# Kernel optimization log

Measured on AMD Instinct MI355X. Metric: run time of the kernel, lower is better.

## Reference

```python
import jax, jax.numpy as jnp
import numpy as np

N, E, FEAT, DIM, B = 200000, 1600000, 128, 64, 256


def setup_inputs() -> dict:
    key = jax.random.key(0)
    ks = jax.random.split(key, 16)
    s = 0.05
    x = jax.random.normal(ks[0], (N, FEAT), jnp.float32)
    edge_index = jax.random.randint(ks[1], (2, E), 0, N)
    batch = jnp.sort(jax.random.randint(ks[2], (N,), 0, B))
    return {
        'x': x,
        'edge_index': edge_index,
        'batch': batch,
        'lin0_w': jax.random.normal(ks[3], (FEAT, DIM), jnp.float32) * s,
        'lin0_b': jax.random.normal(ks[4], (DIM,), jnp.float32) * s,
        'conv_w': jax.random.normal(ks[5], (DIM, DIM), jnp.float32) * s,
        'conv_b': jax.random.normal(ks[6], (DIM,), jnp.float32) * s,
        'gru_w_ih': jax.random.normal(ks[7], (3 * DIM, DIM), jnp.float32) * s,
        'gru_w_hh': jax.random.normal(ks[8], (3 * DIM, DIM), jnp.float32) * s,
        'gru_b_ih': jax.random.normal(ks[9], (3 * DIM,), jnp.float32) * s,
        'gru_b_hh': jax.random.normal(ks[10], (3 * DIM,), jnp.float32) * s,
        'lstm_w_ih': jax.random.normal(ks[11], (4 * DIM, 2 * DIM), jnp.float32) * s,
        'lstm_w_hh': jax.random.normal(ks[12], (4 * DIM, DIM), jnp.float32) * s,
        'lstm_b_ih': jax.random.normal(ks[13], (4 * DIM,), jnp.float32) * s,
        'lstm_b_hh': jax.random.normal(ks[14], (4 * DIM,), jnp.float32) * s,
    }


def reference(x, edge_index, batch, lin0_w, lin0_b, conv_w, conv_b,
              gru_w_ih, gru_w_hh, gru_b_ih, gru_b_hh,
              lstm_w_ih, lstm_w_hh, lstm_b_ih, lstm_b_hh):
    n = x.shape[0]
    d = lin0_w.shape[1]
    # --- GCN normalization with self-loops (PyG gcn_norm, symmetric) ---
    loops = jnp.arange(n)
    row = jnp.concatenate([edge_index[0], loops])  # source nodes
    col = jnp.concatenate([edge_index[1], loops])  # target nodes
    deg = jax.ops.segment_sum(jnp.ones(row.shape, jnp.float32), col, num_segments=N)
    dinv = jnp.where(deg > 0, jax.lax.rsqrt(deg), 0.0)
    norm = dinv[row] * dinv[col]  # [E+N]

    out = jax.nn.relu(x @ lin0_w + lin0_b)  # [N, D]
    h = out  # GRU hidden (layer dim squeezed)
    feat = out
    for _ in range(3):
        # GCNConv: aggregate normalized neighbor messages
        hw = out @ conv_w                                   # [N, D]
        m = jax.ops.segment_sum(norm[:, None] * hw[row], col, num_segments=N) + conv_b
        m = jax.nn.relu(m)
        # torch.nn.GRU cell (gate order: reset, update, new)
        gi = m @ gru_w_ih.T + gru_b_ih
        gh = h @ gru_w_hh.T + gru_b_hh
        ir, iz, in_ = jnp.split(gi, 3, axis=-1)
        hr, hz, hn = jnp.split(gh, 3, axis=-1)
        r = jax.nn.sigmoid(ir + hr)
        z = jax.nn.sigmoid(iz + hz)
        ncand = jnp.tanh(in_ + r * hn)
        h = (1.0 - z) * ncand + z * h
        out = h
        feat = out

    # --- Set2Set pooling, processing_steps=3 (LSTM: 2D -> D) ---
    q_star = jnp.zeros((B, 2 * d), x.dtype)
    hl = jnp.zeros((B, d), x.dtype)
    cl = jnp.zeros((B, d), x.dtype)
    for _ in range(3):
        gates = q_star @ lstm_w_ih.T + lstm_b_ih + hl @ lstm_w_hh.T + lstm_b_hh
        i_, f_, g_, o_ = jnp.split(gates, 4, axis=-1)  # torch order i,f,g,o
        cl = jax.nn.sigmoid(f_) * cl + jax.nn.sigmoid(i_) * jnp.tanh(g_)
        hl = jax.nn.sigmoid(o_) * jnp.tanh(cl)
        q = hl                                             # [B, D]
        e = jnp.sum(out * q[batch], axis=-1)               # [N]
        emax = jax.ops.segment_max(e, batch, num_segments=B)
        a = jnp.exp(e - jax.lax.stop_gradient(emax)[batch])
        denom = jax.ops.segment_sum(a, batch, num_segments=B)
        a = a / denom[batch]                               # scatter-softmax
        r_read = jax.ops.segment_sum(a[:, None] * out, batch, num_segments=B)
        q_star = jnp.concatenate([q, r_read], axis=-1)     # [B, 2D]
    return (q_star, feat)
```

## Files before the change

kernel.cpp:

```cpp
#include <hip/hip_runtime.h>
#include <math.h>

#define FEATD 128
#define DIM 64
#define NB 256
#define SCB 256
#define KB 16
#define RNG 128
#define NBUCKMAX 2048
#define CH1 8192

typedef short bf16x8 __attribute__((ext_vector_type(8)));
typedef float f32x4 __attribute__((ext_vector_type(4)));

__device__ __forceinline__ float frcp_(float x){ return __builtin_amdgcn_rcpf(x); }
__device__ __forceinline__ float sigmoidf_(float x){ return frcp_(1.f+__expf(-x)); }
__device__ __forceinline__ float tanhf_(float x){ float e=__expf(2.f*x); return 1.f-2.f*frcp_(e+1.f); }

__device__ __forceinline__ unsigned short f2bf(float f){
  unsigned u = __float_as_uint(f);
  unsigned r = (u + 0x7FFFu + ((u>>16)&1u)) >> 16;
  return (unsigned short)r;
}
__device__ __forceinline__ float bf2f(unsigned short s){
  return __uint_as_float(((unsigned)s)<<16);
}

__device__ __forceinline__ int lower_bound_i(const int* __restrict__ a, int n, int key){
  int lo=0, hi=n;
  while(lo<hi){ int mid=(lo+hi)>>1; if(a[mid]<key) lo=mid+1; else hi=mid; }
  return lo;
}

__global__ void k_count(const int* __restrict__ col, int* __restrict__ deg, int E){
  int i=blockIdx.x*blockDim.x+threadIdx.x;
  if(i<E) atomicAdd(&deg[col[i]],1);
}

__global__ void k_dinv(const int* __restrict__ deg, float* __restrict__ dinv, int n){
  int i=blockIdx.x*blockDim.x+threadIdx.x;
  if(i<n) dinv[i]=rsqrtf((float)(deg[i]+1));
}

__global__ __launch_bounds__(256) void k_scan_part(const int* __restrict__ deg, int* __restrict__ part, int n){
  __shared__ int s[256];
  int b=blockIdx.x;
  int chunk=(n+SCB-1)/SCB;
  int lo=b*chunk, hi=min(lo+chunk,n);
  int acc=0;
  for(int i=lo+threadIdx.x;i<hi;i+=256) acc+=deg[i];
  s[threadIdx.x]=acc; __syncthreads();
  for(int off=128;off;off>>=1){
    if(threadIdx.x<off) s[threadIdx.x]+=s[threadIdx.x+off];
    __syncthreads();
  }
  if(threadIdx.x==0) part[b]=s[0];
}

__global__ __launch_bounds__(256) void k_scan_mid(int* __restrict__ part){
  __shared__ int s[256];
  int t=threadIdx.x;
  s[t]=part[t]; __syncthreads();
  for(int off=1;off<256;off<<=1){
    int v=(t>=off)? s[t-off]:0;
    __syncthreads();
    s[t]+=v;
    __syncthreads();
  }
  part[t]=(t>0)? s[t-1]:0;
}

__global__ __launch_bounds__(256) void k_scan_out(const int* __restrict__ deg, const int* __restrict__ part,
                                                  int* __restrict__ rp, int* __restrict__ gcur, int n){
  __shared__ int s[256];
  int b=blockIdx.x, t=threadIdx.x;
  int chunk=(n+SCB-1)/SCB;
  int lo=b*chunk, hi=min(lo+chunk,n);
  int tchunk=(chunk+255)/256;
  int tlo=lo+t*tchunk, thi=min(tlo+tchunk,hi);
  int acc=0;
  for(int i=tlo;i<thi;i++) acc+=deg[i];
  s[t]=acc; __syncthreads();
  for(int off=1;off<256;off<<=1){
    int v=(t>=off)? s[t-off]:0;
    __syncthreads();
    s[t]+=v;
    __syncthreads();
  }
  int pre=part[b]+((t>0)? s[t-1]:0);
  for(int i=tlo;i<thi;i++){
    rp[i]=pre;
    if((i&(RNG-1))==0) gcur[(i>>7)*32]=pre;
    pre+=deg[i];
  }
  if(b==SCB-1 && t==0) rp[n]=part[b]+s[255];
}

__global__ __launch_bounds__(256) void k_binscat(const int* __restrict__ row, const int* __restrict__ col,
                       int* __restrict__ gcur, unsigned* __restrict__ tmp, int E, int nbuck){
  __shared__ int lcnt[NBUCKMAX];
  __shared__ int lcur[NBUCKMAX];
  int t=threadIdx.x;
  for(int i=t;i<nbuck;i+=256) lcnt[i]=0;
  __syncthreads();
  int lo=blockIdx.x*CH1, hi=min(lo+CH1,E);
  for(int i=lo+t;i<hi;i+=256) atomicAdd(&lcnt[col[i]>>7],1);
  __syncthreads();
  for(int i=t;i<nbuck;i+=256){
    int cnt=lcnt[i];
    lcur[i]=(cnt>0)? atomicAdd(&gcur[i*32],cnt):0;
  }
  __syncthreads();
  for(int i=lo+t;i<hi;i+=256){
    int c=col[i], r=row[i];
    int pos=atomicAdd(&lcur[c>>7],1);
    tmp[pos]=((unsigned)r<<7)|(unsigned)(c&127);
  }
}

__global__ __launch_bounds__(256) void k_place(const unsigned* __restrict__ tmp, const int* __restrict__ rp,
                      const float* __restrict__ dinv, int2* __restrict__ epack, int n, int nbuck){
  __shared__ int lfill[RNG];
  __shared__ int lrp[RNG];
  __shared__ float ldv[RNG];
  int b=blockIdx.x, t=threadIdx.x;
  int nbase=b*RNG;
  int nn=min(RNG,n-nbase);
  if(t<nn){ lfill[t]=0; lrp[t]=rp[nbase+t]; ldv[t]=dinv[nbase+t]; }
  __syncthreads();
  int lo=rp[nbase], hi=rp[min(nbase+RNG,n)];
  for(int j=lo+t;j<hi;j+=256){
    unsigned v=tmp[j];
    int cl=v&127;
    int r=(int)(v>>7);
    int pos=atomicAdd(&lfill[cl],1);
    epack[lrp[cl]+pos]=make_int2(r,__float_as_int(dinv[r]*ldv[cl]));
  }
}

__global__ void k_prep_plain(const float* __restrict__ W, unsigned short* __restrict__ Bf, int K, int C){
  int i=blockIdx.x*blockDim.x+threadIdx.x;
  if(i>=K*C) return;
  int k=i/C, c=i%C;
  int t=c>>4, s=k>>5, lane=(c&15)|(((k>>3)&3)<<4), r=k&7;
  int S=K>>5;
  Bf[(((t*S)+s)*64+lane)*8+r]=f2bf(W[(size_t)k*C+c]);
}

__global__ void k_prep_gru(const float* __restrict__ wih, const float* __restrict__ whh,
                           unsigned short* __restrict__ Bf){
  int i=blockIdx.x*blockDim.x+threadIdx.x;
  if(i>=128*256) return;
  int k=i>>8, c=i&255;
  float v;
  if(c<128){
    v = (k<64) ? wih[c*64+k] : whh[c*64+(k-64)];
  } else if(c<192){
    v = (k<64) ? wih[c*64+k] : 0.f;
  } else {
    v = (k<64) ? 0.f : whh[(c-64)*64+(k-64)];
  }
  int t=c>>4, s=k>>5, lane=(c&15)|(((k>>3)&3)<<4), r=k&7;
  Bf[(((s*16)+t)*64+lane)*8+r]=f2bf(v);
}

__global__ __launch_bounds__(256) void k_lin0(const float* __restrict__ x, const unsigned short* __restrict__ Bf,
                      const float* __restrict__ bias,
                      unsigned short* __restrict__ hb, int ngrp){
  __shared__ __align__(16) unsigned short lt[4][16][72];
  int l=threadIdx.x&63, w=threadIdx.x>>6;
  int g=blockIdx.x*4+w;
  if(g>=ngrp) return;
  int row16=l&15, koff=(l>>4)*8, l16=l&15;
  f32x4 acc[4]={};
  const float* xr = x + (size_t)(g*16+row16)*128 + koff;
  #pragma unroll
  for(int s=0;s<4;s++){
    f32x4 a0=*(const f32x4*)(xr+s*32);
    f32x4 a1=*(const f32x4*)(xr+s*32+4);
    bf16x8 af;
    #pragma unroll
    for(int r=0;r<4;r++){ af[r]=(short)f2bf(a0[r]); af[4+r]=(short)f2bf(a1[r]); }
    #pragma unroll
    for(int t=0;t<4;t++){
      bf16x8 bf=*(const bf16x8*)(Bf+(((t*4)+s)*64+l)*8);
      acc[t]=__builtin_amdgcn_mfma_f32_16x16x32_bf16(af,bf,acc[t],0,0,0);
    }
  }
  #pragma unroll
  for(int t=0;t<4;t++){
    int c=t*16+l16;
    float b=bias[c];
    #pragma unroll
    for(int j=0;j<4;j++)
      lt[w][(l>>4)*4+j][c]=f2bf(fmaxf(acc[t][j]+b,0.f));
  }
  #pragma unroll
  for(int i=0;i<4;i++){
    int rl=i*4+(l>>4);
    uint2 v=*(const uint2*)&lt[w][rl][l16*4];
    ((uint2*)hb)[(((unsigned)(g*16+rl))<<4)+l16]=v;
  }
}

__global__ __launch_bounds__(256,4) void k_gruagg(
                     const unsigned short* __restrict__ hin, unsigned short* __restrict__ hout,
                     const int* __restrict__ rp, const int2* __restrict__ epack,
                     const float* __restrict__ dinv,
                     const unsigned short* __restrict__ Bcnv, const float* __restrict__ cb,
                     const unsigned short* __restrict__ Bgru,
                     const float* __restrict__ bih, const float* __restrict__ bhh,
                     float* __restrict__ h, int last, int ngrp, int n){
  __shared__ __align__(16) unsigned short Bs[8192];
  __shared__ __align__(16) unsigned short tAH[4][2][16][72];
  int tid=threadIdx.x;
  int l=tid&63, w=tid>>6;
  int g=blockIdx.x*4+w;
  bool act = g<ngrp;
  int gc = act? g : (ngrp-1);
  int q=l>>4, l16=l&15;
  int row16=l&15, koff=(l>>4)*8;

  unsigned short (*tA)[72] = tAH[w][0];
  unsigned short (*tH)[72] = tAH[w][1];

  bf16x8 bc[8];
  #pragma unroll
  for(int f=0;f<8;f++) bc[f]=*(const bf16x8*)(Bcnv+((size_t)f*64+l)*8);

  {
    const f32x4* gh=(const f32x4*)Bgru; f32x4* lh=(f32x4*)Bs;
    #pragma unroll
    for(int i=0;i<4;i++) lh[i*256+tid]=gh[i*256+tid];
  }

  const uint2* h64=(const uint2*)hin;
  #pragma unroll
  for(int rr=0;rr<4;rr++){
    int node=min(gc*16+rr*4+q, n-1);
    float a0=0.f,a1=0.f,a2=0.f,a3=0.f, b0=0.f,b1=0.f,b2=0.f,b3=0.f;
    int s=rp[node], e=rp[node+1];
    uint2 selfp=h64[((unsigned)node<<4)+l16];
    int j=s;
    for(; j+7<e; j+=8){
      int2 e0=epack[j],   e1=epack[j+1], e2=epack[j+2], e3=epack[j+3];
      int2 e4=epack[j+4], e5=epack[j+5], e6=epack[j+6], e7=epack[j+7];
      uint2 p0=h64[((unsigned)e0.x<<4)+l16];
      uint2 p1=h64[((unsigned)e1.x<<4)+l16];
      uint2 p2=h64[((unsigned)e2.x<<4)+l16];
      uint2 p3=h64[((unsigned)e3.x<<4)+l16];
      uint2 p4=h64[((unsigned)e4.x<<4)+l16];
      uint2 p5=h64[((unsigned)e5.x<<4)+l16];
      uint2 p6=h64[((unsigned)e6.x<<4)+l16];
      uint2 p7=h64[((unsigned)e7.x<<4)+l16];
      float n0=__int_as_float(e0.y), n1=__int_as_float(e1.y);
      float n2=__int_as_float(e2.y), n3=__int_as_float(e3.y);
      float n4=__int_as_float(e4.y), n5=__int_as_float(e5.y);
      float n6=__int_as_float(e6.y), n7=__int_as_float(e7.y);
      a0+=n0*bf2f((unsigned short)p0.x); a1+=n0*bf2f((unsigned short)(p0.x>>16));
      a2+=n0*bf2f((unsigned short)p0.y); a3+=n0*bf2f((unsigned short)(p0.y>>16));
      b0+=n1*bf2f((unsigned short)p1.x); b1+=n1*bf2f((unsigned short)(p1.x>>16));
      b2+=n1*bf2f((unsigned short)p1.y); b3+=n1*bf2f((unsigned short)(p1.y>>16));
      a0+=n2*bf2f((unsigned short)p2.x); a1+=n2*bf2f((unsigned short)(p2.x>>16));
      a2+=n2*bf2f((unsigned short)p2.y); a3+=n2*bf2f((unsigned short)(p2.y>>16));
      b0+=n3*bf2f((unsigned short)p3.x); b1+=n3*bf2f((unsigned short)(p3.x>>16));
      b2+=n3*bf2f((unsigned short)p3.y); b3+=n3*bf2f((unsigned short)(p3.y>>16));
      a0+=n4*bf2f((unsigned short)p4.x); a1+=n4*bf2f((unsigned short)(p4.x>>16));
      a2+=n4*bf2f((unsigned short)p4.y); a3+=n4*bf2f((unsigned short)(p4.y>>16));
      b0+=n5*bf2f((unsigned short)p5.x); b1+=n5*bf2f((unsigned short)(p5.x>>16));
      b2+=n5*bf2f((unsigned short)p5.y); b3+=n5*bf2f((unsigned short)(p5.y>>16));
      a0+=n6*bf2f((unsigned short)p6.x); a1+=n6*bf2f((unsigned short)(p6.x>>16));
      a2+=n6*bf2f((unsigned short)p6.y); a3+=n6*bf2f((unsigned short)(p6.y>>16));
      b0+=n7*bf2f((unsigned short)p7.x); b1+=n7*bf2f((unsigned short)(p7.x>>16));
      b2+=n7*bf2f((unsigned short)p7.y); b3+=n7*bf2f((unsigned short)(p7.y>>16));
    }
    for(; j+3<e; j+=4){
      int2 e0=epack[j];
      int2 e1=epack[j+1];
      int2 e2=epack[j+2];
      int2 e3=epack[j+3];
      uint2 p0=h64[((unsigned)e0.x<<4)+l16];
      uint2 p1=h64[((unsigned)e1.x<<4)+l16];
      uint2 p2=h64[((unsigned)e2.x<<4)+l16];
      uint2 p3=h64[((unsigned)e3.x<<4)+l16];
      float n0=__int_as_float(e0.y), n1=__int_as_float(e1.y);
      float n2=__int_as_float(e2.y), n3=__int_as_float(e3.y);
      a0+=n0*bf2f((unsigned short)p0.x); a1+=n0*bf2f((unsigned short)(p0.x>>16));
      a2+=n0*bf2f((unsigned short)p0.y); a3+=n0*bf2f((unsigned short)(p0.y>>16));
      b0+=n1*bf2f((unsigned short)p1.x); b1+=n1*bf2f((unsigned short)(p1.x>>16));
      b2+=n1*bf2f((unsigned short)p1.y); b3+=n1*bf2f((unsigned short)(p1.y>>16));
      a0+=n2*bf2f((unsigned short)p2.x); a1+=n2*bf2f((unsigned short)(p2.x>>16));
      a2+=n2*bf2f((unsigned short)p2.y); a3+=n2*bf2f((unsigned short)(p2.y>>16));
      b0+=n3*bf2f((unsigned short)p3.x); b1+=n3*bf2f((unsigned short)(p3.x>>16));
      b2+=n3*bf2f((unsigned short)p3.y); b3+=n3*bf2f((unsigned short)(p3.y>>16));
    }
    for(; j+1<e; j+=2){
      int2 e0=epack[j];
      int2 e1=epack[j+1];
      uint2 p0=h64[((unsigned)e0.x<<4)+l16];
      uint2 p1=h64[((unsigned)e1.x<<4)+l16];
      float n0=__int_as_float(e0.y), n1=__int_as_float(e1.y);
      a0+=n0*bf2f((unsigned short)p0.x); a1+=n0*bf2f((unsigned short)(p0.x>>16));
      a2+=n0*bf2f((unsigned short)p0.y); a3+=n0*bf2f((unsigned short)(p0.y>>16));
      b0+=n1*bf2f((unsigned short)p1.x); b1+=n1*bf2f((unsigned short)(p1.x>>16));
      b2+=n1*bf2f((unsigned short)p1.y); b3+=n1*bf2f((unsigned short)(p1.y>>16));
    }
    if(j<e){
      int2 e0=epack[j];
      uint2 p0=h64[((unsigned)e0.x<<4)+l16];
      float n0=__int_as_float(e0.y);
      a0+=n0*bf2f((unsigned short)p0.x); a1+=n0*bf2f((unsigned short)(p0.x>>16));
      a2+=n0*bf2f((unsigned short)p0.y); a3+=n0*bf2f((unsigned short)(p0.y>>16));
    }
    float dv=dinv[node]; dv*=dv;
    a0+=b0+dv*bf2f((unsigned short)selfp.x);
    a1+=b1+dv*bf2f((unsigned short)(selfp.x>>16));
    a2+=b2+dv*bf2f((unsigned short)selfp.y);
    a3+=b3+dv*bf2f((unsigned short)(selfp.y>>16));
    int ri=rr*4+q;
    unsigned* tAp=(unsigned*)&tA[ri][l16*4];
    tAp[0]=(unsigned)f2bf(a0)|(((unsigned)f2bf(a1))<<16);
    tAp[1]=(unsigned)f2bf(a2)|(((unsigned)f2bf(a3))<<16);
    unsigned* tHp=(unsigned*)&tH[ri][l16*4];
    tHp[0]=selfp.x; tHp[1]=selfp.y;
  }

  f32x4 accm[4]={};
  #pragma unroll
  for(int s=0;s<2;s++){
    bf16x8 af=*(const bf16x8*)&tA[row16][s*32+koff];
    #pragma unroll
    for(int t=0;t<4;t++)
      accm[t]=__builtin_amdgcn_mfma_f32_16x16x32_bf16(af,bc[t*2+s],accm[t],0,0,0);
  }
  #pragma unroll
  for(int t=0;t<4;t++){
    int c=t*16+l16;
    float b=cb[c];
    #pragma unroll
    for(int j=0;j<4;j++)
      tA[(l>>4)*4+j][c]=f2bf(fmaxf(accm[t][j]+b,0.f));
  }

  f32x4 acc[16]={};
  __syncthreads();
  #pragma unroll
  for(int s=0;s<4;s++){
    if(s>0){
      __syncthreads();
      const f32x4* gh=(const f32x4*)(Bgru+(size_t)s*8192); f32x4* lh=(f32x4*)Bs;
      #pragma unroll
      for(int i=0;i<4;i++) lh[i*256+tid]=gh[i*256+tid];
      __syncthreads();
    }
    bf16x8 af;
    if(s<2) af=*(const bf16x8*)&tA[row16][s*32+koff];
    else    af=*(const bf16x8*)&tH[row16][(s-2)*32+koff];
    #pragma unroll
    for(int t=0;t<16;t++){
      bf16x8 bf=*(const bf16x8*)(Bs+((size_t)t*64+l)*8);
      acc[t]=__builtin_amdgcn_mfma_f32_16x16x32_bf16(af,bf,acc[t],0,0,0);
    }
  }

  if(!act) return;
  float hn[16];
  #pragma unroll
  for(int t=0;t<4;t++){
    int d=t*16+l16;
    float br =bih[d]    +bhh[d];
    float bz =bih[64+d] +bhh[64+d];
    float bni=bih[128+d];
    float bnh=bhh[128+d];
    #pragma unroll
    for(int j=0;j<4;j++){
      float r  = sigmoidf_(acc[t][j]   + br);
      float z  = sigmoidf_(acc[4+t][j] + bz);
      float nc = tanhf_(acc[8+t][j] + bni + r*(acc[12+t][j] + bnh));
      float hold=bf2f(tH[(l>>4)*4+j][d]);
      hn[t*4+j]=(1.f-z)*nc + z*hold;
    }
  }
  #pragma unroll
  for(int t=0;t<4;t++){
    int d=t*16+l16;
    #pragma unroll
    for(int j=0;j<4;j++)
      tH[(l>>4)*4+j][d]=f2bf(hn[t*4+j]);
  }
  #pragma unroll
  for(int i=0;i<4;i++){
    int rl=i*4+(l>>4);
    uint2 v=*(const uint2*)&tH[rl][l16*4];
    ((uint2*)hout)[(((unsigned)(gc*16+rl))<<4)+l16]=v;
  }
  if(last){
    float* ft=(float*)&tAH[w][0][0][0];
    #pragma unroll
    for(int t=0;t<4;t++){
      int d=t*16+l16;
      #pragma unroll
      for(int j=0;j<4;j++)
        ft[((l>>4)*4+j)*68+d]=hn[t*4+j];
    }
    #pragma unroll
    for(int i=0;i<4;i++){
      int rl=i*4+(l>>4);
      f32x4 v=*(const f32x4*)&ft[rl*68+l16*4];
      *(f32x4*)&h[(size_t)(gc*16+rl)*64+l16*4]=v;
    }
  }
}

__global__ __launch_bounds__(256) void k_attn_part(const unsigned short* __restrict__ hb, const int* __restrict__ batch,
                        const float* __restrict__ hl, float* __restrict__ apart, int n){
  int b=blockIdx.x/KB, kb=blockIdx.x%KB;
  int tid=threadIdx.x, lane=tid&63, w=tid>>6;
  __shared__ float qs[64];
  __shared__ float wm[4], wsm[4];
  __shared__ float wacc[4][64];
  if(tid<64) qs[tid]=hl[b*64+tid];
  int lo=lower_bound_i(batch,n,b), hi=lower_bound_i(batch,n,b+1);
  int cnt=hi-lo;
  int chunk=(cnt+KB-1)/KB;
  int slo=lo+kb*chunk, shi=min(slo+chunk,hi);
  __syncthreads();
  float q=qs[lane];
  float mw=-3.0e38f, sw=0.f, aw=0.f;
  for(int i=slo+w;i<shi;i+=4){
    float f=bf2f(hb[(size_t)i*64+lane]);
    float v=f*q;
    #pragma unroll
    for(int off=32;off;off>>=1) v+=__shfl_xor(v,off);
    if(v>mw){
      float sc=__expf(mw-v);
      sw=sw*sc+1.f;
      aw=aw*sc+f;
      mw=v;
    } else {
      float p=__expf(v-mw);
      sw+=p;
      aw+=p*f;
    }
  }
  if(lane==0){ wm[w]=mw; wsm[w]=sw; }
  wacc[w][lane]=aw;
  __syncthreads();
  if(w==0){
    float M=fmaxf(fmaxf(wm[0],wm[1]),fmaxf(wm[2],wm[3]));
    float S=0.f, A=0.f;
    #pragma unroll
    for(int k=0;k<4;k++){
      float sc=__expf(wm[k]-M);
      S+=wsm[k]*sc;
      A+=wacc[k][lane]*sc;
    }
    float* p=apart+(size_t)blockIdx.x*68;
    p[lane]=A;
    if(lane==0){ p[64]=M; p[65]=S; }
  }
}

__global__ __launch_bounds__(256) void k_merge_lstm(const float* __restrict__ apart,
                   float* __restrict__ qstar, float* __restrict__ hl, float* __restrict__ cl,
                   const float* __restrict__ wih, const float* __restrict__ whh,
                   const float* __restrict__ bih, const float* __restrict__ bhh,
                   int do_merge, int do_lstm){
  int b=blockIdx.x, tid=threadIdx.x;
  __shared__ float qs[128];
  __shared__ float gates[256];
  if(do_merge){
    if(tid<64){
      const float* p0=apart+(size_t)b*KB*68;
      float M=-3.0e38f;
      #pragma unroll
      for(int k=0;k<KB;k++) M=fmaxf(M,p0[k*68+64]);
      float S=0.f, A=0.f;
      #pragma unroll
      for(int k=0;k<KB;k++){
        float sc=__expf(p0[k*68+64]-M);
        S+=p0[k*68+65]*sc;
        A+=p0[k*68+tid]*sc;
      }
      float inv=(S>0.f)? 1.f/S:0.f;
      float r=A*inv;
      qs[64+tid]=r;
      qstar[b*128+64+tid]=r;
    }
  } else {
    if(tid<64) qs[64+tid]=qstar[b*128+64+tid];
  }
  if(tid<64) qs[tid]=hl[b*64+tid];
  __syncthreads();
  if(!do_lstm) return;
  float acc=bih[tid]+bhh[tid];
  const float* wi=wih+(size_t)tid*128;
  #pragma unroll 8
  for(int k=0;k<128;k++) acc+=qs[k]*wi[k];
  const float* w2=whh+(size_t)tid*64;
  #pragma unroll 8
  for(int k=0;k<64;k++) acc+=qs[k]*w2[k];
  gates[tid]=acc;
  __syncthreads();
  if(tid<64){
    float i_=gates[tid], f_=gates[64+tid], g_=gates[128+tid], o_=gates[192+tid];
    float c=sigmoidf_(f_)*cl[b*64+tid]+sigmoidf_(i_)*tanhf(g_);
    float hn=sigmoidf_(o_)*tanhf(c);
    cl[b*64+tid]=c; hl[b*64+tid]=hn;
    qstar[b*128+tid]=hn;
  }
}

extern "C" void kernel_launch(void* const* d_in, const int* in_sizes, int n_in,
                              void* d_out, int out_size, void* d_ws, size_t ws_size,
                              hipStream_t stream){
  const float* x      =(const float*)d_in[0];
  const int*   ei     =(const int*)d_in[1];
  const int*   batch  =(const int*)d_in[2];
  const float* lin0_w =(const float*)d_in[3];
  const float* lin0_b =(const float*)d_in[4];
  const float* conv_w =(const float*)d_in[5];
  const float* conv_b =(const float*)d_in[6];
  const float* gwih   =(const float*)d_in[7];
  const float* gwhh   =(const float*)d_in[8];
  const float* gbih   =(const float*)d_in[9];
  const float* gbhh   =(const float*)d_in[10];
  const float* lwih   =(const float*)d_in[11];
  const float* lwhh   =(const float*)d_in[12];
  const float* lbih   =(const float*)d_in[13];
  const float* lbhh   =(const float*)d_in[14];

  int N = in_sizes[0]/FEATD;
  int E = in_sizes[1]/2;
  const int* row = ei;
  const int* col = ei + E;

  float* qstar = (float*)d_out;
  float* h     = (float*)d_out + NB*2*DIM;

  char* ws=(char*)d_ws;
  size_t off=0;
  auto alloc=[&](size_t bytes)->void*{ void* p=ws+off; off=(off+bytes+255)&~(size_t)255; return p; };
  int*   deg  =(int*)  alloc((size_t)N*4);
  float* dinv =(float*)alloc((size_t)N*4);
  int*   rp   =(int*)  alloc((size_t)(N+1)*4);
  int*   part =(int*)  alloc((size_t)SCB*4);
  int*   gcur =(int*)  alloc((size_t)NBUCKMAX*32*4);
  unsigned* tmp=(unsigned*)alloc((size_t)E*4);
  int2*  epack=(int2*) alloc((size_t)E*8);
  unsigned short* hb0  =(unsigned short*)alloc((size_t)N*64*2);
  unsigned short* hb1  =(unsigned short*)alloc((size_t)N*64*2);
  float* hl   =(float*)alloc((size_t)NB*DIM*4);
  float* cl   =(float*)alloc((size_t)NB*DIM*4);
  float* apart=(float*)alloc((size_t)NB*KB*68*4);
  unsigned short* Bgru =(unsigned short*)alloc(128*256*2);
  unsigned short* Blin =(unsigned short*)alloc(128*64*2);
  unsigned short* Bcnv =(unsigned short*)alloc(64*64*2);

  hipMemsetAsync(deg ,0,(size_t)N*4,stream);
  hipMemsetAsync(hl  ,0,(size_t)NB*DIM*4,stream);
  hipMemsetAsync(cl  ,0,(size_t)NB*DIM*4,stream);
  hipMemsetAsync(qstar,0,(size_t)NB*2*DIM*4,stream);

  int nbuck=(N+RNG-1)/RNG;

  k_count<<<(E+255)/256,256,0,stream>>>(col,deg,E);
  k_dinv <<<(N+255)/256,256,0,stream>>>(deg,dinv,N);
  k_scan_part<<<SCB,256,0,stream>>>(deg,part,N);
  k_scan_mid <<<1,256,0,stream>>>(part);
  k_scan_out <<<SCB,256,0,stream>>>(deg,part,rp,gcur,N);
  k_binscat<<<(E+CH1-1)/CH1,256,0,stream>>>(row,col,gcur,tmp,E,nbuck);
  k_place<<<nbuck,256,0,stream>>>(tmp,rp,dinv,epack,N,nbuck);

  k_prep_plain<<<(128*64+255)/256,256,0,stream>>>(lin0_w,Blin,128,64);
  k_prep_plain<<<(64*64+255)/256,256,0,stream>>>(conv_w,Bcnv,64,64);
  k_prep_gru  <<<(128*256+255)/256,256,0,stream>>>(gwih,gwhh,Bgru);

  int ngrp=(N+15)/16;
  int gb=(ngrp+3)/4;

  k_lin0<<<gb,256,0,stream>>>(x,Blin,lin0_b,hb0,ngrp);

  k_gruagg<<<gb,256,0,stream>>>(hb0,hb1,rp,epack,dinv,Bcnv,conv_b,Bgru,gbih,gbhh,h,0,ngrp,N);
  k_gruagg<<<gb,256,0,stream>>>(hb1,hb0,rp,epack,dinv,Bcnv,conv_b,Bgru,gbih,gbhh,h,0,ngrp,N);
  k_gruagg<<<gb,256,0,stream>>>(hb0,hb1,rp,epack,dinv,Bcnv,conv_b,Bgru,gbih,gbhh,h,1,ngrp,N);

  k_merge_lstm<<<NB,256,0,stream>>>(apart,qstar,hl,cl,lwih,lwhh,lbih,lbhh,0,1);
  for(int st=0;st<3;st++){
    k_attn_part<<<NB*KB,256,0,stream>>>(hb1,batch,hl,apart,N);
    int do_lstm = (st<2)? 1:0;
    k_merge_lstm<<<NB,256,0,stream>>>(apart,qstar,hl,cl,lwih,lwhh,lbih,lbhh,1,do_lstm);
  }
}
```

Measured before the change: 541.5 us.

## Restructure GRU GEMM by output tile to cut registers and raise occupancy

The fused aggregation+GRU kernel now computes gate outputs one 16-column tile at a time: the GRU weights are re-laid out so each tile's r/z/n gates sit in consecutive chunks, and the LDS staging buffer is halved. This drops the 16 live accumulator vectors to 4, moves the conv weight loads into a scoped block, and raises launch bounds from 4 to 6 waves per SIMD to improve latency hiding in the gather phase. It also folds the dinv computation into the scan-partition kernel, removing one launch. The cost is twice as many block-wide syncs and reloads of LDS weight chunks (8 stages instead of 4).

```diff
diff --git a/kernel.cpp b/kernel.cpp
--- a/kernel.cpp
+++ b/kernel.cpp
@@ -37,18 +37,18 @@
   if(i<E) atomicAdd(&deg[col[i]],1);
 }
 
-__global__ void k_dinv(const int* __restrict__ deg, float* __restrict__ dinv, int n){
-  int i=blockIdx.x*blockDim.x+threadIdx.x;
-  if(i<n) dinv[i]=rsqrtf((float)(deg[i]+1));
-}
-
-__global__ __launch_bounds__(256) void k_scan_part(const int* __restrict__ deg, int* __restrict__ part, int n){
+__global__ __launch_bounds__(256) void k_scan_part(const int* __restrict__ deg, int* __restrict__ part,
+                                                   float* __restrict__ dinv, int n){
   __shared__ int s[256];
   int b=blockIdx.x;
   int chunk=(n+SCB-1)/SCB;
   int lo=b*chunk, hi=min(lo+chunk,n);
   int acc=0;
-  for(int i=lo+threadIdx.x;i<hi;i+=256) acc+=deg[i];
+  for(int i=lo+threadIdx.x;i<hi;i+=256){
+    int d=deg[i];
+    acc+=d;
+    dinv[i]=rsqrtf((float)(d+1));
+  }
   s[threadIdx.x]=acc; __syncthreads();
   for(int off=128;off;off>>=1){
     if(threadIdx.x<off) s[threadIdx.x]+=s[threadIdx.x+off];
@@ -161,7 +161,9 @@
     v = (k<64) ? 0.f : whh[(c-64)*64+(k-64)];
   }
   int t=c>>4, s=k>>5, lane=(c&15)|(((k>>3)&3)<<4), r=k&7;
-  Bf[(((s*16)+t)*64+lane)*8+r]=f2bf(v);
+  int jt=t&3, gate=t>>2;
+  int f=jt*16 + (s>>1)*8 + gate*2 + (s&1);
+  Bf[((size_t)f*64+lane)*8+r]=f2bf(v);
 }
 
 __global__ __launch_bounds__(256) void k_lin0(const float* __restrict__ x, const unsigned short* __restrict__ Bf,
@@ -203,7 +205,7 @@
   }
 }
 
-__global__ __launch_bounds__(256,4) void k_gruagg(
+__global__ __launch_bounds__(256,6) void k_gruagg(
                      const unsigned short* __restrict__ hin, unsigned short* __restrict__ hout,
                      const int* __restrict__ rp, const int2* __restrict__ epack,
                      const float* __restrict__ dinv,
@@ -211,7 +213,7 @@
                      const unsigned short* __restrict__ Bgru,
                      const float* __restrict__ bih, const float* __restrict__ bhh,
                      float* __restrict__ h, int last, int ngrp, int n){
-  __shared__ __align__(16) unsigned short Bs[8192];
+  __shared__ __align__(16) unsigned short Bs[4096];
   __shared__ __align__(16) unsigned short tAH[4][2][16][72];
   int tid=threadIdx.x;
   int l=tid&63, w=tid>>6;
@@ -224,14 +226,10 @@
   unsigned short (*tA)[72] = tAH[w][0];
   unsigned short (*tH)[72] = tAH[w][1];
 
-  bf16x8 bc[8];
-  #pragma unroll
-  for(int f=0;f<8;f++) bc[f]=*(const bf16x8*)(Bcnv+((size_t)f*64+l)*8);
-
   {
     const f32x4* gh=(const f32x4*)Bgru; f32x4* lh=(f32x4*)Bs;
-    #pragma unroll
-    for(int i=0;i<4;i++) lh[i*256+tid]=gh[i*256+tid];
+    lh[tid]=gh[tid];
+    lh[256+tid]=gh[256+tid];
   }
 
   const uint2* h64=(const uint2*)hin;
@@ -325,62 +323,72 @@
     tHp[0]=selfp.x; tHp[1]=selfp.y;
   }
 
-  f32x4 accm[4]={};
+  {
+    bf16x8 bc[8];
+    #pragma unroll
+    for(int f=0;f<8;f++) bc[f]=*(const bf16x8*)(Bcnv+((size_t)f*64+l)*8);
+    f32x4 accm[4]={};
+    #pragma unroll
+    for(int s=0;s<2;s++){
+      bf16x8 af=*(const bf16x8*)&tA[row16][s*32+koff];
+      #pragma unroll
+      for(int t=0;t<4;t++)
+        accm[t]=__builtin_amdgcn_mfma_f32_16x16x32_bf16(af,bc[t*2+s],accm[t],0,0,0);
+    }
+    #pragma unroll
+    for(int t=0;t<4;t++){
+      int c=t*16+l16;
+      float b=cb[c];
+      #pragma unroll
+      for(int j=0;j<4;j++)
+        tA[(l>>4)*4+j][c]=f2bf(fmaxf(accm[t][j]+b,0.f));
+    }
+  }
+
+  float hn[16];
+  __syncthreads();
   #pragma unroll
-  for(int s=0;s<2;s++){
-    bf16x8 af=*(const bf16x8*)&tA[row16][s*32+koff];
-    #pragma unroll
-    for(int t=0;t<4;t++)
-      accm[t]=__builtin_amdgcn_mfma_f32_16x16x32_bf16(af,bc[t*2+s],accm[t],0,0,0);
-  }
-  #pragma unroll
-  for(int t=0;t<4;t++){
-    int c=t*16+l16;
-    float b=cb[c];
-    #pragma unroll
-    for(int j=0;j<4;j++)
-      tA[(l>>4)*4+j][c]=f2bf(fmaxf(accm[t][j]+b,0.f));
-  }
-
-  f32x4 acc[16]={};
-  __syncthreads();
-  #pragma unroll
-  for(int s=0;s<4;s++){
-    if(s>0){
-      __syncthreads();
-      const f32x4* gh=(const f32x4*)(Bgru+(size_t)s*8192); f32x4* lh=(f32x4*)Bs;
+  for(int jt=0;jt<4;jt++){
+    f32x4 acc[4]={};
+    #pragma unroll
+    for(int sh=0;sh<2;sh++){
+      int c=jt*2+sh;
+      if(c>0){
+        __syncthreads();
+        const f32x4* gh=(const f32x4*)(Bgru+(size_t)c*4096); f32x4* lh=(f32x4*)Bs;
+        lh[tid]=gh[tid];
+        lh[256+tid]=gh[256+tid];
+        __syncthreads();
+      }
       #pragma unroll
-      for(int i=0;i<4;i++) lh[i*256+tid]=gh[i*256+tid];
-      __syncthreads();
-    }
-    bf16x8 af;
-    if(s<2) af=*(const bf16x8*)&tA[row16][s*32+koff];
-    else    af=*(const bf16x8*)&tH[row16][(s-2)*32+koff];
-    #pragma unroll
-    for(int t=0;t<16;t++){
-      bf16x8 bf=*(const bf16x8*)(Bs+((size_t)t*64+l)*8);
-      acc[t]=__builtin_amdgcn_mfma_f32_16x16x32_bf16(af,bf,acc[t],0,0,0);
-    }
-  }
-
-  if(!act) return;
-  float hn[16];
-  #pragma unroll
-  for(int t=0;t<4;t++){
-    int d=t*16+l16;
+      for(int s01=0;s01<2;s01++){
+        int s=sh*2+s01;
+        bf16x8 af;
+        if(s<2) af=*(const bf16x8*)&tA[row16][s*32+koff];
+        else    af=*(const bf16x8*)&tH[row16][(s-2)*32+koff];
+        #pragma unroll
+        for(int gt=0;gt<4;gt++){
+          bf16x8 bf=*(const bf16x8*)(Bs+((size_t)(gt*2+s01)*64+l)*8);
+          acc[gt]=__builtin_amdgcn_mfma_f32_16x16x32_bf16(af,bf,acc[gt],0,0,0);
+        }
+      }
+    }
+    int d=jt*16+l16;
     float br =bih[d]    +bhh[d];
     float bz =bih[64+d] +bhh[64+d];
     float bni=bih[128+d];
     float bnh=bhh[128+d];
     #pragma unroll
-    for(int j=0;j<4;j++){
-      float r  = sigmoidf_(acc[t][j]   + br);
-      float z  = sigmoidf_(acc[4+t][j] + bz);
-      float nc = tanhf_(acc[8+t][j] + bni + r*(acc[12+t][j] + bnh));
-      float hold=bf2f(tH[(l>>4)*4+j][d]);
-      hn[t*4+j]=(1.f-z)*nc + z*hold;
-    }
-  }
+    for(int jj=0;jj<4;jj++){
+      float r  = sigmoidf_(acc[0][jj] + br);
+      float z  = sigmoidf_(acc[1][jj] + bz);
+      float nc = tanhf_(acc[2][jj] + bni + r*(acc[3][jj] + bnh));
+      float hold=bf2f(tH[(l>>4)*4+jj][d]);
+      hn[jt*4+jj]=(1.f-z)*nc + z*hold;
+    }
+  }
+
+  if(!act) return;
   #pragma unroll
   for(int t=0;t<4;t++){
     int d=t*16+l16;
@@ -565,8 +573,7 @@
   int nbuck=(N+RNG-1)/RNG;
 
   k_count<<<(E+255)/256,256,0,stream>>>(col,deg,E);
-  k_dinv <<<(N+255)/256,256,0,stream>>>(deg,dinv,N);
-  k_scan_part<<<SCB,256,0,stream>>>(deg,part,N);
+  k_scan_part<<<SCB,256,0,stream>>>(deg,part,dinv,N);
   k_scan_mid <<<1,256,0,stream>>>(part);
   k_scan_out <<<SCB,256,0,stream>>>(deg,part,rp,gcur,N);
   k_binscat<<<(E+CH1-1)/CH1,256,0,stream>>>(row,col,gcur,tmp,E,nbuck);
```

After: 652.2 us (median of 2 runs). 1.2x slower.
